# Kernel tuning notes

Hardware: AMD Instinct MI355X
Metric: run time of the kernel (lower is better)

Reference implementation:

```python
import jax, jax.numpy as jnp
import numpy as np

B, T, E, H = 1024, 200, 128, 128
N_ITEMS, N_CATS = 100000, 1000
LN_EPS = 1e-5


def _prelu(x, a):
    return jnp.where(x >= 0, x, a * x)


def _layernorm(x, g, b):
    m = x.mean(-1, keepdims=True)
    v = ((x - m) ** 2).mean(-1, keepdims=True)
    return (x - m) / jnp.sqrt(v + LN_EPS) * g + b


def setup_inputs() -> dict:
    key = jax.random.key(0)
    it = iter(jax.random.split(key, 64))
    nx = lambda: next(it)
    def lin(out_d, in_d):
        s = 1.0 / np.sqrt(in_d)
        return jax.random.uniform(nx(), (out_d, in_d), jnp.float32, -s, s)
    inp = {}
    inp['behavior_ids'] = jax.random.randint(nx(), (B, T), 0, N_ITEMS)
    inp['candidate_id'] = jax.random.randint(nx(), (B,), 0, N_ITEMS)
    inp['candidate_cat'] = jax.random.randint(nx(), (B,), 0, N_CATS)
    inp['dense_features'] = jax.random.normal(nx(), (B, 5), jnp.float32)
    inp['item_emb'] = (jax.random.normal(nx(), (N_ITEMS, E), jnp.float32) * 0.01).at[0].set(0.0)
    inp['cat_emb'] = (jax.random.normal(nx(), (N_CATS, E // 2), jnp.float32) * 0.01).at[0].set(0.0)
    # nn.GRU params (gate order r,z,n)
    inp['gru_wih'] = lin(3 * H, E)
    inp['gru_whh'] = lin(3 * H, H)
    inp['gru_bih'] = jnp.zeros((3 * H,), jnp.float32)
    inp['gru_bhh'] = jnp.zeros((3 * H,), jnp.float32)
    # auxiliary_net: Linear(H,E) -> ReLU -> Linear(E,1)
    inp['aux_w1'] = lin(E, H); inp['aux_b1'] = jnp.zeros((E,), jnp.float32)
    inp['aux_w2'] = lin(1, E); inp['aux_b2'] = jnp.zeros((1,), jnp.float32)
    # attention_mlp: Linear(3H,64) -> PReLU -> Linear(64,1)
    inp['att_w1'] = lin(64, 3 * H); inp['att_b1'] = jnp.zeros((64,), jnp.float32)
    inp['att_a'] = jnp.array(0.25, jnp.float32)
    inp['att_w2'] = lin(1, 64); inp['att_b2'] = jnp.zeros((1,), jnp.float32)
    # AUGRU gates: Linear(2H, H) each
    inp['wz'] = lin(H, 2 * H); inp['bz'] = jnp.zeros((H,), jnp.float32)
    inp['wr'] = lin(H, 2 * H); inp['br'] = jnp.zeros((H,), jnp.float32)
    inp['wh'] = lin(H, 2 * H); inp['bh'] = jnp.zeros((H,), jnp.float32)
    # dense_proj Linear(5,32)
    inp['dp_w'] = lin(32, 5); inp['dp_b'] = jnp.zeros((32,), jnp.float32)
    # MLP: 352 -> 256 -> 128 -> 64, each Linear + LayerNorm + PReLU
    dims = [H + E + E // 2 + 32, 256, 128, 64]
    for i in range(3):
        inp[f'm_w{i+1}'] = lin(dims[i + 1], dims[i])
        inp[f'm_b{i+1}'] = jnp.zeros((dims[i + 1],), jnp.float32)
        inp[f'ln_g{i+1}'] = jnp.ones((dims[i + 1],), jnp.float32)
        inp[f'ln_b{i+1}'] = jnp.zeros((dims[i + 1],), jnp.float32)
        inp[f'pa{i+1}'] = jnp.array(0.25, jnp.float32)
    # 3 task heads Linear(64,1), stacked
    inp['heads_w'] = lin(3, 64); inp['heads_b'] = jnp.zeros((3,), jnp.float32)
    return inp


def _forward_core(behavior_ids, candidate_id, candidate_cat, dense_features,
                  item_emb, cat_emb, gru_wih, gru_whh, gru_bih, gru_bhh,
                  aux_w1, aux_b1, aux_w2, aux_b2,
                  att_w1, att_b1, att_a, att_w2, att_b2,
                  wz, bz, wr, br, wh, bh, dp_w, dp_b,
                  m_w1, m_b1, ln_g1, ln_b1, pa1,
                  m_w2, m_b2, ln_g2, ln_b2, pa2,
                  m_w3, m_b3, ln_g3, ln_b3, pa3,
                  heads_w, heads_b):
    beh = item_emb[behavior_ids]            # [B,T,E]
    cand = item_emb[candidate_id]           # [B,E]
    catv = cat_emb[candidate_cat]           # [B,E//2]
    Bsz = beh.shape[0]
    Hd = gru_whh.shape[1]
    h0 = jnp.zeros((Bsz, Hd), beh.dtype)
    # --- interest extractor GRU (cuDNN GRU math, gate order r,z,n) ---
    xp = jnp.einsum('bte,ge->btg', beh, gru_wih) + gru_bih  # [B,T,3H]
    def gru_step(h, x):
        hp = h @ gru_whh.T + gru_bhh
        xr, xz, xn = jnp.split(x, 3, -1)
        hr, hz, hn = jnp.split(hp, 3, -1)
        r = jax.nn.sigmoid(xr + hr)
        z = jax.nn.sigmoid(xz + hz)
        n = jnp.tanh(xn + r * hn)
        hnew = (1 - z) * n + z * h
        return hnew, hnew
    _, hs = jax.lax.scan(gru_step, h0, jnp.swapaxes(xp, 0, 1))
    hs = jnp.swapaxes(hs, 0, 1)             # [B,T,H]
    # --- auxiliary logits ---
    aux = jax.nn.relu(hs[:, :-1] @ aux_w1.T + aux_b1) @ aux_w2.T + aux_b2  # [B,T-1,1]
    # --- attention (embed_dim == hidden_size so cand_proj == candidate_emb) ---
    ce = cand[:, None, :]
    att_in = jnp.concatenate([hs, jnp.broadcast_to(ce, hs.shape), hs * ce], -1)  # [B,T,3H]
    scores = (_prelu(att_in @ att_w1.T + att_b1, att_a) @ att_w2.T + att_b2)[..., 0]
    att = jax.nn.softmax(scores, axis=-1)   # [B,T]
    # --- AUGRU: attention-modulated update gate ---
    def augru_step(h, xs):
        x, a = xs                           # x: [B,H], a: [B]
        comb = jnp.concatenate([x, h], -1)
        z = jax.nn.sigmoid(comb @ wz.T + bz)
        r = jax.nn.sigmoid(comb @ wr.T + br)
        comb_r = jnp.concatenate([x, r * h], -1)
        ht = jnp.tanh(comb_r @ wh.T + bh)
        zp = a[:, None] * z
        return (1 - zp) * h + zp * ht, None
    hT, _ = jax.lax.scan(augru_step, h0, (jnp.swapaxes(hs, 0, 1), att.T))
    # --- fusion MLP (dropout is identity in eval) ---
    dense_out = dense_features @ dp_w.T + dp_b
    x = jnp.concatenate([hT, cand, catv, dense_out], -1)  # [B,352]
    for (w, b, g, be, a) in ((m_w1, m_b1, ln_g1, ln_b1, pa1),
                             (m_w2, m_b2, ln_g2, ln_b2, pa2),
                             (m_w3, m_b3, ln_g3, ln_b3, pa3)):
        x = _prelu(_layernorm(x @ w.T + b, g, be), a)
    preds = jax.nn.sigmoid(x @ heads_w.T + heads_b)  # [B,3] == 3 heads of [B,1]
    return preds, aux


def reference(behavior_ids, candidate_id, candidate_cat, dense_features,
              item_emb, cat_emb, gru_wih, gru_whh, gru_bih, gru_bhh,
              aux_w1, aux_b1, aux_w2, aux_b2,
              att_w1, att_b1, att_a, att_w2, att_b2,
              wz, bz, wr, br, wh, bh, dp_w, dp_b,
              m_w1, m_b1, ln_g1, ln_b1, pa1,
              m_w2, m_b2, ln_g2, ln_b2, pa2,
              m_w3, m_b3, ln_g3, ln_b3, pa3,
              heads_w, heads_b):
    return _forward_core(behavior_ids, candidate_id, candidate_cat, dense_features,
                         item_emb, cat_emb, gru_wih, gru_whh, gru_bih, gru_bhh,
                         aux_w1, aux_b1, aux_w2, aux_b2,
                         att_w1, att_b1, att_a, att_w2, att_b2,
                         wz, bz, wr, br, wh, bh, dp_w, dp_b,
                         m_w1, m_b1, ln_g1, ln_b1, pa1,
                         m_w2, m_b2, ln_g2, ln_b2, pa2,
                         m_w3, m_b3, ln_g3, ln_b3, pa3,
                         heads_w, heads_b)
```

## Files before the change

kernel.cpp:

```cpp
#include <hip/hip_runtime.h>


typedef __bf16 bf16;
typedef float f32x4 __attribute__((ext_vector_type(4)));
typedef __bf16 bf16x8 __attribute__((ext_vector_type(8)));
typedef __bf16 bf16x4 __attribute__((ext_vector_type(4)));

#define MFMA16(a, b, c) __builtin_amdgcn_mfma_f32_16x16x32_bf16((a), (b), (c), 0, 0, 0)

#define BATCH 1024
#define SEQT 200
#define F32_ONE 0x3F800000u

__device__ __forceinline__ float sigm(float x) {
  return __builtin_amdgcn_rcpf(1.0f + __expf(-x));
}
__device__ __forceinline__ float tanh_fast(float x) {
  float ax = fabsf(x);
  float t = 1.0f - 2.0f * __builtin_amdgcn_rcpf(__expf(2.0f * ax) + 1.0f);
  return copysignf(t, x);
}

__device__ __forceinline__ void bar_lgkm() {
  asm volatile("s_waitcnt lgkmcnt(0)\n\ts_barrier" ::: "memory");
}

__device__ __forceinline__ void dma16(const void* g, void* l) {
  __builtin_amdgcn_global_load_lds((__attribute__((address_space(1))) void*)g,
                                   (__attribute__((address_space(3))) void*)l,
                                   16, 0, 0);
}

template <typename DT> __device__ __forceinline__ float ldf(const DT* p, long i);
template <> __device__ __forceinline__ float ldf<bf16>(const bf16* p, long i) { return (float)p[i]; }
template <> __device__ __forceinline__ float ldf<float>(const float* p, long i) { return p[i]; }

template <typename DT> __device__ __forceinline__ bf16x8 ld8(const DT* p, long i);
template <> __device__ __forceinline__ bf16x8 ld8<bf16>(const bf16* p, long i) {
  return *(const bf16x8*)(p + i);
}
template <> __device__ __forceinline__ bf16x8 ld8<float>(const float* p, long i) {
  f32x4 a = *(const f32x4*)(p + i);
  f32x4 b = *(const f32x4*)(p + i + 4);
  bf16x8 r;
  r[0] = (bf16)a[0]; r[1] = (bf16)a[1]; r[2] = (bf16)a[2]; r[3] = (bf16)a[3];
  r[4] = (bf16)b[0]; r[5] = (bf16)b[1]; r[6] = (bf16)b[2]; r[7] = (bf16)b[3];
  return r;
}

template <typename DT>
__device__ __forceinline__ void cast_body(const DT* __restrict__ src, bf16* __restrict__ dst) {
  const long i = ((long)blockIdx.x * 256 + threadIdx.x) * 8;
  if (i < 100000L * 128) *(bf16x8*)(dst + i) = ld8(src, i);
}
__global__ __launch_bounds__(256) void k_cast(
    const unsigned* __restrict__ disc, const void* src, bf16* dst) {
  if (*disc == F32_ONE) cast_body<float>((const float*)src, dst);
  else                  cast_body<bf16>((const bf16*)src, dst);
}

template <typename DT>
__device__ __forceinline__ void prep_body(
    const int* __restrict__ cid, const int* __restrict__ ccat,
    const DT* __restrict__ dense, const DT* __restrict__ item_emb,
    const DT* __restrict__ cat_emb, const DT* __restrict__ dp_w,
    const DT* __restrict__ dp_b, bf16* __restrict__ candbuf, bf16* __restrict__ xf) {
  const int b = blockIdx.x;
  const int t = threadIdx.x;
  bf16 v = (bf16)ldf(item_emb, (long)cid[b] * 128 + t);
  candbuf[b * 128 + t] = v;
  xf[(long)b * 352 + 128 + t] = v;
  if (t < 64) xf[(long)b * 352 + 256 + t] = (bf16)ldf(cat_emb, (long)ccat[b] * 64 + t);
  if (t < 32) {
    float s = ldf(dp_b, t);
    for (int k = 0; k < 5; k++) s += ldf(dense, b * 5 + k) * ldf(dp_w, t * 5 + k);
    xf[(long)b * 352 + 320 + t] = (bf16)s;
  }
}
__global__ __launch_bounds__(128) void k_prep(
    const unsigned* __restrict__ disc, const int* cid, const int* ccat,
    const void* dense, const void* item_emb, const void* cat_emb,
    const void* dp_w, const void* dp_b, bf16* candbuf, bf16* xf) {
  if (*disc == F32_ONE)
    prep_body<float>(cid, ccat, (const float*)dense, (const float*)item_emb,
                     (const float*)cat_emb, (const float*)dp_w, (const float*)dp_b, candbuf, xf);
  else
    prep_body<bf16>(cid, ccat, (const bf16*)dense, (const bf16*)item_emb,
                    (const bf16*)cat_emb, (const bf16*)dp_w, (const bf16*)dp_b, candbuf, xf);
}

template <typename DT>
__device__ __forceinline__ void gru5_body(
    const int* __restrict__ ids, const bf16* __restrict__ ieb,
    const DT* __restrict__ wih, const DT* __restrict__ whh,
    const DT* __restrict__ bih, const DT* __restrict__ bhh, bf16* __restrict__ hs,
    bf16 (*hA)[16][136], bf16 (*xb)[4][16][128]) {
  const int b0 = blockIdx.x * 16;
  const int tid = threadIdx.x;
  const int w = tid >> 6, lane = tid & 63, l15 = lane & 15, quad = lane >> 4;
  const int nc = w * 16 + l15;

  for (int i = tid; i < 2 * 16 * 136; i += 512) ((bf16*)hA)[i] = (bf16)0.0f;

  bf16x8 wir[4], wiz[4], win_[4], whr[4], whz[4], whn[4];
#pragma unroll
  for (int k = 0; k < 4; k++) {
    const long off = k * 32 + quad * 8;
    wir[k] = ld8(wih, (long)nc * 128 + off);
    wiz[k] = ld8(wih, (long)(128 + nc) * 128 + off);
    win_[k] = ld8(wih, (long)(256 + nc) * 128 + off);
    whr[k] = ld8(whh, (long)nc * 128 + off);
    whz[k] = ld8(whh, (long)(128 + nc) * 128 + off);
    whn[k] = ld8(whh, (long)(256 + nc) * 128 + off);
  }
  const float br_s = ldf(bih, nc) + ldf(bhh, nc);
  const float bz_s = ldf(bih, 128 + nc) + ldf(bhh, 128 + nc);
  const float bxn_s = ldf(bih, 256 + nc);
  const float bhn_s = ldf(bhh, 256 + nc);

  const int idrow = (tid >> 4) & 15;
  const int* idbase = ids + (long)(b0 + idrow) * SEQT;
  const int srcoff = ((tid & 15) ^ (idrow & 7)) * 8;

  auto DMA = [&](const int4 id4, int buf) {
#pragma unroll
    for (int j = 0; j < 2; j++) {
      const int slot = j * 2 + (tid >> 8);
      dma16(ieb + (long)((&id4.x)[slot]) * 128 + srcoff,
            (char*)&xb[buf][0][0][0] + (j * 512 + tid) * 16);
    }
  };

  const int srow = tid >> 5, sch = (tid & 31) * 4;
  bf16* hsb = hs + ((long)(b0 + srow) * SEQT) * 128 + sch;

  float hreg[4] = {0.f, 0.f, 0.f, 0.f};
  const f32x4 z4 = {0.f, 0.f, 0.f, 0.f};

  int4 idv = *(const int4*)(idbase);
  DMA(idv, 0);
  idv = *(const int4*)(idbase + 4);
  asm volatile("s_waitcnt vmcnt(1)" ::: "memory");
  __builtin_amdgcn_sched_barrier(0);
  __builtin_amdgcn_s_barrier();

#define GRU_STEP(P, S, WAITC)                                                  \
  {                                                                            \
    const int tt = t0 + (S);                                                   \
    bf16x8 af[4], xaf[4];                                                      \
    _Pragma("unroll") for (int k = 0; k < 4; k++) {                            \
      af[k] = *(const bf16x8*)&hA[P][l15][k * 32 + quad * 8];                  \
      xaf[k] = *(const bf16x8*)((const char*)&xb[buf][S][0][0] + l15 * 256 +   \
                                ((((k << 2) + quad) ^ (l15 & 7)) << 4));       \
    }                                                                          \
    { const int slot = tt ? tt - 1 : 0;                                        \
      bf16x4 hv = *(const bf16x4*)&hA[P][srow][sch];                           \
      *(bf16x4*)(hsb + (long)slot * 128) = hv; }                               \
    f32x4 ar = z4, az = z4, axn = z4, ahn = z4;                                \
    _Pragma("unroll") for (int k = 0; k < 4; k++) {                            \
      ar = MFMA16(xaf[k], wir[k], ar);                                         \
      az = MFMA16(xaf[k], wiz[k], az);                                         \
      axn = MFMA16(xaf[k], win_[k], axn);                                      \
    }                                                                          \
    _Pragma("unroll") for (int k = 0; k < 4; k++) {                            \
      ar = MFMA16(af[k], whr[k], ar);                                          \
      az = MFMA16(af[k], whz[k], az);                                          \
      ahn = MFMA16(af[k], whn[k], ahn);                                        \
    }                                                                          \
    _Pragma("unroll") for (int r = 0; r < 4; r++) {                            \
      float r_ = sigm(ar[r] + br_s);                                           \
      float z_ = sigm(az[r] + bz_s);                                           \
      float n_ = tanh_fast(axn[r] + bxn_s + r_ * (ahn[r] + bhn_s));            \
      float hnew = (1.0f - z_) * n_ + z_ * hreg[r];                            \
      hreg[r] = hnew;                                                          \
      hA[(P) ^ 1][quad * 4 + r][nc] = (bf16)hnew;                              \
    }                                                                          \
    if (WAITC) {                                                               \
       \
      asm volatile("s_waitcnt vmcnt(5) lgkmcnt(0)\n\ts_barrier" ::: "memory"); \
    } else {                                                                   \
      bar_lgkm();                                                              \
    }                                                                          \
  }

  for (int c = 0; c < 50; c++) {
    const int t0 = c * 4;
    const int buf = c & 1;
    if (c < 49) {
      DMA(idv, buf ^ 1);
      int nid = (c + 2) * 4; if (nid > 196) nid = 196;
      idv = *(const int4*)(idbase + nid);
    }
    GRU_STEP(0, 0, 0) GRU_STEP(1, 1, 0) GRU_STEP(0, 2, 0) GRU_STEP(1, 3, (c < 49))
  }
#undef GRU_STEP
  { bf16x4 hv = *(const bf16x4*)&hA[0][srow][sch];
    *(bf16x4*)(hsb + (long)(SEQT - 1) * 128) = hv; }
}
__global__ __launch_bounds__(512, 1) void k_gru5(
    const unsigned* __restrict__ disc, const int* ids, const bf16* ieb,
    const void* wih, const void* whh, const void* bih, const void* bhh, bf16* hs) {
  __shared__ __align__(16) bf16 hA[2][16][136];
  __shared__ __align__(16) bf16 xb[2][4][16][128];
  if (*disc == F32_ONE)
    gru5_body<float>(ids, ieb, (const float*)wih, (const float*)whh,
                     (const float*)bih, (const float*)bhh, hs, hA, xb);
  else
    gru5_body<bf16>(ids, ieb, (const bf16*)wih, (const bf16*)whh,
                    (const bf16*)bih, (const bf16*)bhh, hs, hA, xb);
}

template <typename DT>
__device__ __forceinline__ void attaux_body(
    const bf16* __restrict__ hs, const int* __restrict__ cid,
    const DT* __restrict__ item_emb,
    const DT* __restrict__ aw1, const DT* __restrict__ ab1,
    const DT* __restrict__ aw2, const DT* __restrict__ ab2,
    const DT* __restrict__ tw1, const DT* __restrict__ tb1, const DT* __restrict__ ta,
    const DT* __restrict__ tw2, const DT* __restrict__ tb2,
    float* __restrict__ sc, float* __restrict__ outaux,
    bf16 (*As)[64][128], float (*scPt)[64], float (*scPa)[64]) {
  const int t0 = blockIdx.x * 64;
  const int b0 = blockIdx.y * 16;
  const int tid = threadIdx.x, w = tid >> 6, lane = tid & 63, l15 = lane & 15, quad = lane >> 4;

  const int tn = w * 16 + l15;
  bf16x8 wth[4], wtc[4], wthc[4], wa0[4], wa1[4];
#pragma unroll
  for (int k = 0; k < 4; k++) {
    const long off = k * 32 + quad * 8;
    wth[k]  = ld8(tw1, (long)tn * 384 + off);
    wtc[k]  = ld8(tw1, (long)tn * 384 + 128 + off);
    wthc[k] = ld8(tw1, (long)tn * 384 + 256 + off);
    wa0[k]  = ld8(aw1, (long)((2 * w) * 16 + l15) * 128 + off);
    wa1[k]  = ld8(aw1, (long)((2 * w + 1) * 16 + l15) * 128 + off);
  }
  const float tb1c = ldf(tb1, tn), tw2c = ldf(tw2, tn);
  const float ab1c0 = ldf(ab1, (2 * w) * 16 + l15), aw2c0 = ldf(aw2, (2 * w) * 16 + l15);
  const float ab1c1 = ldf(ab1, (2 * w + 1) * 16 + l15), aw2c1 = ldf(aw2, (2 * w + 1) * 16 + l15);
  const float aP = ldf(ta, 0), tb2s = ldf(tb2, 0), ab2s = ldf(ab2, 0);

  auto DMA = [&](int b, int buf) {
#pragma unroll
    for (int c = 0; c < 4; c++) {
      const int idx = c * 256 + tid;
      const int row = idx >> 4, p = idx & 15;
      int t = t0 + row; if (t > SEQT - 1) t = SEQT - 1;
      const bf16* src = hs + ((long)b * SEQT + t) * 128 + ((p ^ (row & 7)) * 8);
      dma16(src, (char*)(&As[buf][0][0]) + idx * 16);
    }
  };
  auto CANDLD = [&](int b, bf16x8* cf) {
#pragma unroll
    for (int k = 0; k < 4; k++)
      cf[k] = ld8(item_emb, (long)cid[b] * 128 + k * 32 + quad * 8);
  };

  const f32x4 z4 = {0.f, 0.f, 0.f, 0.f};
  bf16x8 candA[4], candB[4];
  DMA(b0, 0);
  CANDLD(b0, candA);
  asm volatile("s_waitcnt vmcnt(0)" ::: "memory");
  __builtin_amdgcn_sched_barrier(0);
  __builtin_amdgcn_s_barrier();

#define AA_STEP(BI, CUSE, CPF)                                                 \
  {                                                                            \
    const int b = b0 + (BI);                                                   \
    const int buf = (BI) & 1;                                                  \
    if ((BI) + 1 < 16) { DMA(b + 1, buf ^ 1); CANDLD(b + 1, CPF); }            \
    _Pragma("unroll") for (int m = 0; m < 4; m++) {                            \
      const bf16* arow = &As[buf][m * 16 + l15][0];                            \
      bf16x8 af[4], hcf[4];                                                    \
      _Pragma("unroll") for (int k = 0; k < 4; k++)                            \
        af[k] = *(const bf16x8*)((const char*)arow +                           \
                                 (((k * 4 + quad) ^ (l15 & 7)) << 4));         \
      _Pragma("unroll") for (int k = 0; k < 4; k++)                            \
      _Pragma("unroll") for (int j = 0; j < 8; j++)                            \
        hcf[k][j] = (bf16)((float)af[k][j] * (float)CUSE[k][j]);               \
      f32x4 at = z4, aa0 = z4, aa1 = z4;                                       \
      _Pragma("unroll") for (int k = 0; k < 4; k++) {                          \
        at = MFMA16(af[k], wth[k], at);                                        \
        at = MFMA16(CUSE[k], wtc[k], at);                                      \
        at = MFMA16(hcf[k], wthc[k], at);                                      \
        aa0 = MFMA16(af[k], wa0[k], aa0);                                      \
        aa1 = MFMA16(af[k], wa1[k], aa1);                                      \
      }                                                                        \
      float tp[4], ap[4];                                                      \
      _Pragma("unroll") for (int r = 0; r < 4; r++) {                          \
        float y = at[r] + tb1c;                                                \
        y = (y >= 0.f) ? y : aP * y;                                           \
        tp[r] = y * tw2c;                                                      \
        float y0 = aa0[r] + ab1c0;                                             \
        float y1 = aa1[r] + ab1c1;                                             \
        ap[r] = (y0 > 0.f ? y0 : 0.f) * aw2c0 + (y1 > 0.f ? y1 : 0.f) * aw2c1; \
      }                                                                        \
      _Pragma("unroll") for (int mm = 1; mm < 16; mm <<= 1)                    \
      _Pragma("unroll") for (int r = 0; r < 4; r++) {                          \
        tp[r] += __shfl_xor(tp[r], mm, 64);                                    \
        ap[r] += __shfl_xor(ap[r], mm, 64);                                    \
      }                                                                        \
      if (l15 == 0) {                                                          \
        *(float4*)&scPt[w][m * 16 + quad * 4] =                                \
            make_float4(tp[0], tp[1], tp[2], tp[3]);                           \
        *(float4*)&scPa[w][m * 16 + quad * 4] =                                \
            make_float4(ap[0], ap[1], ap[2], ap[3]);                           \
      }                                                                        \
    }                                                                          \
    bar_lgkm();                                                                \
    if (tid < 64) {                                                            \
      int t = t0 + tid;                                                        \
      if (t < SEQT) {                                                          \
        float s = scPt[0][tid] + scPt[1][tid] + scPt[2][tid] + scPt[3][tid];   \
        sc[(long)b * SEQT + t] = s + tb2s;                                     \
      }                                                                        \
    } else if (tid < 128) {                                                    \
      int tt2 = tid - 64, t = t0 + tt2;                                        \
      if (t < SEQT - 1) {                                                      \
        float s = scPa[0][tt2] + scPa[1][tt2] + scPa[2][tt2] + scPa[3][tt2];   \
        outaux[(long)b * 199 + t] = s + ab2s;                                  \
      }                                                                        \
    }                                                                          \
    asm volatile("s_waitcnt vmcnt(0) lgkmcnt(0)" ::: "memory");                \
    __builtin_amdgcn_sched_barrier(0);                                         \
    __builtin_amdgcn_s_barrier();                                              \
  }

  for (int bi = 0; bi < 16; bi += 2) {
    AA_STEP(bi, candA, candB)
    AA_STEP(bi + 1, candB, candA)
  }
#undef AA_STEP
}
__global__ __launch_bounds__(256, 1) void k_attaux(
    const unsigned* __restrict__ disc, const bf16* hs, const int* cid,
    const void* item_emb,
    const void* aw1, const void* ab1, const void* aw2, const void* ab2,
    const void* tw1, const void* tb1, const void* ta, const void* tw2, const void* tb2,
    float* sc, float* outaux) {
  __shared__ __align__(16) bf16 As[2][64][128];
  __shared__ __align__(16) float scPt[4][64];
  __shared__ __align__(16) float scPa[4][64];
  if (*disc == F32_ONE)
    attaux_body<float>(hs, cid, (const float*)item_emb,
                       (const float*)aw1, (const float*)ab1, (const float*)aw2, (const float*)ab2,
                       (const float*)tw1, (const float*)tb1, (const float*)ta,
                       (const float*)tw2, (const float*)tb2, sc, outaux, As, scPt, scPa);
  else
    attaux_body<bf16>(hs, cid, (const bf16*)item_emb,
                      (const bf16*)aw1, (const bf16*)ab1, (const bf16*)aw2, (const bf16*)ab2,
                      (const bf16*)tw1, (const bf16*)tb1, (const bf16*)ta,
                      (const bf16*)tw2, (const bf16*)tb2, sc, outaux, As, scPt, scPa);
}

__global__ __launch_bounds__(256) void k_softmax(float* __restrict__ sc) {
  const int b = blockIdx.x, tid = threadIdx.x;
  __shared__ float red[256];
  float v = (tid < SEQT) ? sc[(long)b * SEQT + tid] : -1e30f;
  red[tid] = v; __syncthreads();
  for (int s = 128; s > 0; s >>= 1) { if (tid < s) red[tid] = fmaxf(red[tid], red[tid + s]); __syncthreads(); }
  float mx = red[0]; __syncthreads();
  float e = (tid < SEQT) ? __expf(v - mx) : 0.f;
  red[tid] = e; __syncthreads();
  for (int s = 128; s > 0; s >>= 1) { if (tid < s) red[tid] += red[tid + s]; __syncthreads(); }
  float inv = 1.0f / red[0];
  if (tid < SEQT) sc[(long)b * SEQT + tid] = e * inv;
}

template <typename DT>
__device__ __forceinline__ void augru5_body(
    const bf16* __restrict__ hsrc, const float* __restrict__ att,
    const DT* __restrict__ wz, const DT* __restrict__ wr, const DT* __restrict__ wh,
    const DT* __restrict__ bzv, const DT* __restrict__ brv, const DT* __restrict__ bhv,
    bf16* __restrict__ xf_out,
    bf16 (*hA)[16][136], bf16 (*rhA)[136], float (*attL)[201],
    bf16 (*xb)[4][16][128]) {
  const int b0 = blockIdx.x * 16;
  const int tid = threadIdx.x;
  const int w = tid >> 6, lane = tid & 63, l15 = lane & 15, quad = lane >> 4;
  const int nc = w * 16 + l15;

  for (int i = tid; i < 2 * 16 * 136; i += 512) ((bf16*)hA)[i] = (bf16)0.0f;
  for (int i = tid; i < 16 * SEQT; i += 512) {
    int r = i / SEQT, c = i - r * SEQT;
    attL[r][c] = att[(long)(b0 + r) * SEQT + c];
  }

  bf16x8 wzx[4], wzh[4], wrx[4], wrh[4], whx[4], whh_[4];
#pragma unroll
  for (int k = 0; k < 4; k++) {
    const long off = k * 32 + quad * 8;
    wzx[k] = ld8(wz, (long)nc * 256 + off);
    wzh[k] = ld8(wz, (long)nc * 256 + 128 + off);
    wrx[k] = ld8(wr, (long)nc * 256 + off);
    wrh[k] = ld8(wr, (long)nc * 256 + 128 + off);
    whx[k] = ld8(wh, (long)nc * 256 + off);
    whh_[k] = ld8(wh, (long)nc * 256 + 128 + off);
  }
  const float bz_s = ldf(bzv, nc);
  const float br_s = ldf(brv, nc);
  const float bh_s = ldf(bhv, nc);

  const int drow = (tid >> 4) & 15;
  const int srcoff = ((tid & 15) ^ (drow & 7)) * 8;
  auto DMA = [&](int t0, int buf) {
#pragma unroll
    for (int j = 0; j < 2; j++) {
      const int slot = j * 2 + (tid >> 8);
      dma16(hsrc + ((long)(b0 + drow) * SEQT + t0 + slot) * 128 + srcoff,
            (char*)&xb[buf][0][0][0] + (j * 512 + tid) * 16);
    }
  };

  float hreg[4] = {0.f, 0.f, 0.f, 0.f};
  const f32x4 z4 = {0.f, 0.f, 0.f, 0.f};

  DMA(0, 0);
  asm volatile("s_waitcnt vmcnt(0)" ::: "memory");
  __builtin_amdgcn_sched_barrier(0);
  __builtin_amdgcn_s_barrier();

#define AUGRU_STEP(P, S, WAITC)                                                \
  {                                                                            \
    const int tt = t0 + (S);                                                   \
    bf16x8 af[4], xaf[4];                                                      \
    _Pragma("unroll") for (int k = 0; k < 4; k++) {                            \
      af[k] = *(const bf16x8*)&hA[P][l15][k * 32 + quad * 8];                  \
      xaf[k] = *(const bf16x8*)((const char*)&xb[buf][S][0][0] + l15 * 256 +   \
                                ((((k << 2) + quad) ^ (l15 & 7)) << 4));       \
    }                                                                          \
    f32x4 az = z4, ar = z4, axh = z4;                                          \
    _Pragma("unroll") for (int k = 0; k < 4; k++) {                            \
      az = MFMA16(xaf[k], wzx[k], az);                                         \
      ar = MFMA16(xaf[k], wrx[k], ar);                                         \
      axh = MFMA16(xaf[k], whx[k], axh);                                       \
    }                                                                          \
    _Pragma("unroll") for (int k = 0; k < 4; k++) {                            \
      az = MFMA16(af[k], wzh[k], az);                                          \
      ar = MFMA16(af[k], wrh[k], ar);                                          \
    }                                                                          \
    float zp[4];                                                               \
    _Pragma("unroll") for (int r = 0; r < 4; r++) {                            \
      float a_ = attL[quad * 4 + r][tt];                                       \
      float z_ = sigm(az[r] + bz_s);                                           \
      float r_ = sigm(ar[r] + br_s);                                           \
      zp[r] = a_ * z_;                                                         \
      rhA[quad * 4 + r][nc] = (bf16)(r_ * hreg[r]);                            \
    }                                                                          \
    bar_lgkm();                                                                \
    bf16x8 rf[4];                                                              \
    _Pragma("unroll") for (int k = 0; k < 4; k++)                              \
      rf[k] = *(const bf16x8*)&rhA[l15][k * 32 + quad * 8];                    \
    f32x4 ahh = axh;                                                           \
    _Pragma("unroll") for (int k = 0; k < 4; k++)                              \
      ahh = MFMA16(rf[k], whh_[k], ahh);                                       \
    _Pragma("unroll") for (int r = 0; r < 4; r++) {                            \
      float ht = tanh_fast(ahh[r] + bh_s);                                     \
      float hnew = (1.f - zp[r]) * hreg[r] + zp[r] * ht;                       \
      hreg[r] = hnew;                                                          \
      hA[(P) ^ 1][quad * 4 + r][nc] = (bf16)hnew;                              \
    }                                                                          \
    if (WAITC) {                                                               \
                     \
      asm volatile("s_waitcnt vmcnt(0) lgkmcnt(0)\n\ts_barrier" ::: "memory"); \
    } else {                                                                   \
      bar_lgkm();                                                              \
    }                                                                          \
  }

  for (int c = 0; c < 50; c++) {
    const int t0 = c * 4;
    const int buf = c & 1;
    if (c < 49) DMA((c + 1) * 4, buf ^ 1);
    AUGRU_STEP(0, 0, 0) AUGRU_STEP(1, 1, 0) AUGRU_STEP(0, 2, 0) AUGRU_STEP(1, 3, (c < 49))
  }
#undef AUGRU_STEP
#pragma unroll
  for (int r = 0; r < 4; r++)
    xf_out[(long)(b0 + quad * 4 + r) * 352 + nc] = (bf16)hreg[r];
}
__global__ __launch_bounds__(512, 1) void k_augru5(
    const unsigned* __restrict__ disc, const bf16* hsrc, const float* att,
    const void* wz, const void* wr, const void* wh,
    const void* bzv, const void* brv, const void* bhv, bf16* xf_out) {
  __shared__ __align__(16) bf16 hA[2][16][136];
  __shared__ __align__(16) bf16 rhA[16][136];
  __shared__ __align__(16) float attL[16][201];
  __shared__ __align__(16) bf16 xb[2][4][16][128];
  if (*disc == F32_ONE)
    augru5_body<float>(hsrc, att, (const float*)wz, (const float*)wr, (const float*)wh,
                       (const float*)bzv, (const float*)brv, (const float*)bhv, xf_out,
                       hA, rhA, attL, xb);
  else
    augru5_body<bf16>(hsrc, att, (const bf16*)wz, (const bf16*)wr, (const bf16*)wh,
                      (const bf16*)bzv, (const bf16*)brv, (const bf16*)bhv, xf_out,
                      hA, rhA, attL, xb);
}

template <typename DT>
__device__ __forceinline__ void mlp_body(
    const bf16* __restrict__ xf,
    const DT* __restrict__ w1, const DT* __restrict__ b1, const DT* __restrict__ g1, const DT* __restrict__ be1, const DT* __restrict__ pa1,
    const DT* __restrict__ w2, const DT* __restrict__ b2, const DT* __restrict__ g2, const DT* __restrict__ be2, const DT* __restrict__ pa2,
    const DT* __restrict__ w3, const DT* __restrict__ b3, const DT* __restrict__ g3, const DT* __restrict__ be3, const DT* __restrict__ pa3,
    const DT* __restrict__ hw, const DT* __restrict__ hb, float* __restrict__ preds,
    float (*xs)[352], float (*ys)[256]) {
  const int tid = threadIdx.x, w = tid >> 6, lane = tid & 63;
  const int b = blockIdx.x * 4 + w;
  for (int i = lane; i < 352; i += 64) xs[w][i] = (float)xf[(long)b * 352 + i];
  __syncthreads();
  float acc1[4];
#pragma unroll
  for (int oi = 0; oi < 4; oi++) {
    int o = lane + 64 * oi;
    float s = ldf(b1, o);
    for (int k = 0; k < 352; k += 8) {
      bf16x8 wv = ld8(w1, (long)o * 352 + k);
#pragma unroll
      for (int j = 0; j < 8; j++) s += xs[w][k + j] * (float)wv[j];
    }
    acc1[oi] = s;
  }
  float sm = acc1[0] + acc1[1] + acc1[2] + acc1[3];
#pragma unroll
  for (int m = 1; m < 64; m <<= 1) sm += __shfl_xor(sm, m, 64);
  float mean = sm * (1.0f / 256.0f);
  float vs = 0.f;
#pragma unroll
  for (int oi = 0; oi < 4; oi++) { float d = acc1[oi] - mean; vs += d * d; }
#pragma unroll
  for (int m = 1; m < 64; m <<= 1) vs += __shfl_xor(vs, m, 64);
  float rstd = rsqrtf(vs * (1.0f / 256.0f) + 1e-5f);
  float a1 = ldf(pa1, 0);
#pragma unroll
  for (int oi = 0; oi < 4; oi++) {
    int o = lane + 64 * oi;
    float y = (acc1[oi] - mean) * rstd * ldf(g1, o) + ldf(be1, o);
    ys[w][o] = (y >= 0.f) ? y : a1 * y;
  }
  __syncthreads();
  float acc2[2];
#pragma unroll
  for (int oi = 0; oi < 2; oi++) {
    int o = lane + 64 * oi;
    float s = ldf(b2, o);
    for (int k = 0; k < 256; k += 8) {
      bf16x8 wv = ld8(w2, (long)o * 256 + k);
#pragma unroll
      for (int j = 0; j < 8; j++) s += ys[w][k + j] * (float)wv[j];
    }
    acc2[oi] = s;
  }
  sm = acc2[0] + acc2[1];
#pragma unroll
  for (int m = 1; m < 64; m <<= 1) sm += __shfl_xor(sm, m, 64);
  mean = sm * (1.0f / 128.0f);
  vs = 0.f;
#pragma unroll
  for (int oi = 0; oi < 2; oi++) { float d = acc2[oi] - mean; vs += d * d; }
#pragma unroll
  for (int m = 1; m < 64; m <<= 1) vs += __shfl_xor(vs, m, 64);
  rstd = rsqrtf(vs * (1.0f / 128.0f) + 1e-5f);
  float a2 = ldf(pa2, 0);
  __syncthreads();
#pragma unroll
  for (int oi = 0; oi < 2; oi++) {
    int o = lane + 64 * oi;
    float y = (acc2[oi] - mean) * rstd * ldf(g2, o) + ldf(be2, o);
    xs[w][o] = (y >= 0.f) ? y : a2 * y;
  }
  __syncthreads();
  float s3 = ldf(b3, lane);
  for (int k = 0; k < 128; k += 8) {
    bf16x8 wv = ld8(w3, (long)lane * 128 + k);
#pragma unroll
    for (int j = 0; j < 8; j++) s3 += xs[w][k + j] * (float)wv[j];
  }
  sm = s3;
#pragma unroll
  for (int m = 1; m < 64; m <<= 1) sm += __shfl_xor(sm, m, 64);
  mean = sm * (1.0f / 64.0f);
  float d3 = s3 - mean;
  vs = d3 * d3;
#pragma unroll
  for (int m = 1; m < 64; m <<= 1) vs += __shfl_xor(vs, m, 64);
  rstd = rsqrtf(vs * (1.0f / 64.0f) + 1e-5f);
  float a3 = ldf(pa3, 0);
  float y3 = d3 * rstd * ldf(g3, lane) + ldf(be3, lane);
  y3 = (y3 >= 0.f) ? y3 : a3 * y3;
  ys[w][lane] = y3;
  __syncthreads();
  if (lane < 3) {
    float s = ldf(hb, lane);
    for (int k = 0; k < 64; k++) s += ys[w][k] * ldf(hw, lane * 64 + k);
    preds[(long)b * 3 + lane] = sigm(s);
  }
}
__global__ __launch_bounds__(256) void k_mlp(
    const unsigned* __restrict__ disc, const bf16* xf,
    const void* w1, const void* b1, const void* g1, const void* be1, const void* pa1,
    const void* w2, const void* b2, const void* g2, const void* be2, const void* pa2,
    const void* w3, const void* b3, const void* g3, const void* be3, const void* pa3,
    const void* hw, const void* hb, float* preds) {
  __shared__ float xs[4][352];
  __shared__ float ys[4][256];
  if (*disc == F32_ONE)
    mlp_body<float>(xf,
        (const float*)w1, (const float*)b1, (const float*)g1, (const float*)be1, (const float*)pa1,
        (const float*)w2, (const float*)b2, (const float*)g2, (const float*)be2, (const float*)pa2,
        (const float*)w3, (const float*)b3, (const float*)g3, (const float*)be3, (const float*)pa3,
        (const float*)hw, (const float*)hb, preds, xs, ys);
  else
    mlp_body<bf16>(xf,
        (const bf16*)w1, (const bf16*)b1, (const bf16*)g1, (const bf16*)be1, (const bf16*)pa1,
        (const bf16*)w2, (const bf16*)b2, (const bf16*)g2, (const bf16*)be2, (const bf16*)pa2,
        (const bf16*)w3, (const bf16*)b3, (const bf16*)g3, (const bf16*)be3, (const bf16*)pa3,
        (const bf16*)hw, (const bf16*)hb, preds, xs, ys);
}

extern "C" void kernel_launch(void* const* d_in, const int* in_sizes, int n_in,
                              void* d_out, int out_size, void* d_ws, size_t ws_size,
                              hipStream_t stream) {
  const int* behavior_ids = (const int*)d_in[0];
  const int* candidate_id = (const int*)d_in[1];
  const int* candidate_cat = (const int*)d_in[2];
  const void* dense = d_in[3];
  const void* item_emb = d_in[4];
  const void* cat_emb = d_in[5];
  const void* gru_wih = d_in[6];
  const void* gru_whh = d_in[7];
  const void* gru_bih = d_in[8];
  const void* gru_bhh = d_in[9];
  const void* aux_w1 = d_in[10];
  const void* aux_b1 = d_in[11];
  const void* aux_w2 = d_in[12];
  const void* aux_b2 = d_in[13];
  const void* att_w1 = d_in[14];
  const void* att_b1 = d_in[15];
  const void* att_a = d_in[16];
  const void* att_w2 = d_in[17];
  const void* att_b2 = d_in[18];
  const void* wz = d_in[19];
  const void* bz = d_in[20];
  const void* wr = d_in[21];
  const void* br = d_in[22];
  const void* wh = d_in[23];
  const void* bh = d_in[24];
  const void* dp_w = d_in[25];
  const void* dp_b = d_in[26];
  const void* m_w1 = d_in[27];
  const void* m_b1 = d_in[28];
  const void* ln_g1 = d_in[29];
  const void* ln_b1 = d_in[30];
  const void* pa1 = d_in[31];
  const void* m_w2 = d_in[32];
  const void* m_b2 = d_in[33];
  const void* ln_g2 = d_in[34];
  const void* ln_b2 = d_in[35];
  const void* pa2 = d_in[36];
  const void* m_w3 = d_in[37];
  const void* m_b3 = d_in[38];
  const void* ln_g3 = d_in[39];
  const void* ln_b3 = d_in[40];
  const void* pa3 = d_in[41];
  const void* heads_w = d_in[42];
  const void* heads_b = d_in[43];
  (void)in_sizes; (void)n_in; (void)out_size; (void)ws_size;

  const unsigned* disc = (const unsigned*)ln_g1;

  char* ws = (char*)d_ws;
  bf16* HS = (bf16*)(ws);
  float* SC = (float*)(ws + 52428800L);
  bf16* CAND = (bf16*)(ws + 53248000L);
  bf16* XF = (bf16*)(ws + 53510144L);
  bf16* IEB = (bf16*)(ws + 54231040L);
  float* OUT = (float*)d_out;

  k_cast<<<6250, 256, 0, stream>>>(disc, item_emb, IEB);
  k_prep<<<BATCH, 128, 0, stream>>>(disc, candidate_id, candidate_cat, dense, item_emb,
                                    cat_emb, dp_w, dp_b, CAND, XF);
  k_gru5<<<64, 512, 0, stream>>>(disc, behavior_ids, IEB, gru_wih, gru_whh,
                                 gru_bih, gru_bhh, HS);
  k_attaux<<<dim3(4, 64), 256, 0, stream>>>(disc, HS, candidate_id, item_emb,
                                            aux_w1, aux_b1, aux_w2, aux_b2,
                                            att_w1, att_b1, att_a, att_w2, att_b2,
                                            SC, OUT + 3072);
  k_softmax<<<BATCH, 256, 0, stream>>>(SC);
  k_augru5<<<64, 512, 0, stream>>>(disc, HS, SC, wz, wr, wh, bz, br, bh, XF);
  k_mlp<<<256, 256, 0, stream>>>(disc, XF,
      m_w1, m_b1, ln_g1, ln_b1, pa1,
      m_w2, m_b2, ln_g2, ln_b2, pa2,
      m_w3, m_b3, ln_g3, ln_b3, pa3,
      heads_w, heads_b, OUT);
}
```

Before: 733.9 us.

## Precompute next-step input projections in GRU/AUGRU and merge init kernels

In both the GRU and AUGRU recurrences, the input-projection MFMAs for step t+1 are issued right after step t's gate math, so they can overlap with the hidden-state dependency chain instead of sitting on the serial critical path. The cast and prep kernels are merged into one launch, and the unused candidate buffer is dropped. In the attention/aux kernel, the per-block barrier waits with vmcnt(4) instead of a full vmcnt(0) drain when more blocks follow. This costs extra live accumulator registers and adds risk if the partial vmcnt wait does not match the outstanding load count.

```diff
diff --git a/kernel.cpp b/kernel.cpp
--- a/kernel.cpp
+++ b/kernel.cpp
@@ -49,48 +49,43 @@
 }
 
 template <typename DT>
-__device__ __forceinline__ void cast_body(const DT* __restrict__ src, bf16* __restrict__ dst) {
-  const long i = ((long)blockIdx.x * 256 + threadIdx.x) * 8;
-  if (i < 100000L * 128) *(bf16x8*)(dst + i) = ld8(src, i);
-}
-__global__ __launch_bounds__(256) void k_cast(
-    const unsigned* __restrict__ disc, const void* src, bf16* dst) {
-  if (*disc == F32_ONE) cast_body<float>((const float*)src, dst);
-  else                  cast_body<bf16>((const bf16*)src, dst);
+__device__ __forceinline__ void init_body(
+    const DT* __restrict__ item_emb, bf16* __restrict__ ieb,
+    const int* __restrict__ cid, const int* __restrict__ ccat,
+    const DT* __restrict__ dense, const DT* __restrict__ cat_emb,
+    const DT* __restrict__ dp_w, const DT* __restrict__ dp_b,
+    bf16* __restrict__ xf) {
+  if (blockIdx.x < 6250) {
+    const long i = ((long)blockIdx.x * 256 + threadIdx.x) * 8;
+    if (i < 100000L * 128) *(bf16x8*)(ieb + i) = ld8(item_emb, i);
+    return;
+  }
+  const int b = blockIdx.x - 6250;
+  const int t = threadIdx.x;
+  if (t < 128) {
+    xf[(long)b * 352 + 128 + t] = (bf16)ldf(item_emb, (long)cid[b] * 128 + t);
+    if (t < 64) xf[(long)b * 352 + 256 + t] = (bf16)ldf(cat_emb, (long)ccat[b] * 64 + t);
+    if (t < 32) {
+      float s = ldf(dp_b, t);
+      for (int k = 0; k < 5; k++) s += ldf(dense, b * 5 + k) * ldf(dp_w, t * 5 + k);
+      xf[(long)b * 352 + 320 + t] = (bf16)s;
+    }
+  }
+}
+__global__ __launch_bounds__(256) void k_init(
+    const unsigned* __restrict__ disc, const void* item_emb, bf16* ieb,
+    const int* cid, const int* ccat, const void* dense, const void* cat_emb,
+    const void* dp_w, const void* dp_b, bf16* xf) {
+  if (*disc == F32_ONE)
+    init_body<float>((const float*)item_emb, ieb, cid, ccat, (const float*)dense,
+                     (const float*)cat_emb, (const float*)dp_w, (const float*)dp_b, xf);
+  else
+    init_body<bf16>((const bf16*)item_emb, ieb, cid, ccat, (const bf16*)dense,
+                    (const bf16*)cat_emb, (const bf16*)dp_w, (const bf16*)dp_b, xf);
 }
 
 template <typename DT>
-__device__ __forceinline__ void prep_body(
-    const int* __restrict__ cid, const int* __restrict__ ccat,
-    const DT* __restrict__ dense, const DT* __restrict__ item_emb,
-    const DT* __restrict__ cat_emb, const DT* __restrict__ dp_w,
-    const DT* __restrict__ dp_b, bf16* __restrict__ candbuf, bf16* __restrict__ xf) {
-  const int b = blockIdx.x;
-  const int t = threadIdx.x;
-  bf16 v = (bf16)ldf(item_emb, (long)cid[b] * 128 + t);
-  candbuf[b * 128 + t] = v;
-  xf[(long)b * 352 + 128 + t] = v;
-  if (t < 64) xf[(long)b * 352 + 256 + t] = (bf16)ldf(cat_emb, (long)ccat[b] * 64 + t);
-  if (t < 32) {
-    float s = ldf(dp_b, t);
-    for (int k = 0; k < 5; k++) s += ldf(dense, b * 5 + k) * ldf(dp_w, t * 5 + k);
-    xf[(long)b * 352 + 320 + t] = (bf16)s;
-  }
-}
-__global__ __launch_bounds__(128) void k_prep(
-    const unsigned* __restrict__ disc, const int* cid, const int* ccat,
-    const void* dense, const void* item_emb, const void* cat_emb,
-    const void* dp_w, const void* dp_b, bf16* candbuf, bf16* xf) {
-  if (*disc == F32_ONE)
-    prep_body<float>(cid, ccat, (const float*)dense, (const float*)item_emb,
-                     (const float*)cat_emb, (const float*)dp_w, (const float*)dp_b, candbuf, xf);
-  else
-    prep_body<bf16>(cid, ccat, (const bf16*)dense, (const bf16*)item_emb,
-                    (const bf16*)cat_emb, (const bf16*)dp_w, (const bf16*)dp_b, candbuf, xf);
-}
-
-template <typename DT>
-__device__ __forceinline__ void gru5_body(
+__device__ __forceinline__ void gru9_body(
     const int* __restrict__ ids, const bf16* __restrict__ ieb,
     const DT* __restrict__ wih, const DT* __restrict__ whh,
     const DT* __restrict__ bih, const DT* __restrict__ bhh, bf16* __restrict__ hs,
@@ -118,9 +113,9 @@
   const float bxn_s = ldf(bih, 256 + nc);
   const float bhn_s = ldf(bhh, 256 + nc);
 
-  const int idrow = (tid >> 4) & 15;
-  const int* idbase = ids + (long)(b0 + idrow) * SEQT;
-  const int srcoff = ((tid & 15) ^ (idrow & 7)) * 8;
+  const int drow = (tid >> 4) & 15;
+  const int* idbase = ids + (long)(b0 + drow) * SEQT;
+  const int srcoff = ((tid & 15) ^ (drow & 7)) * 8;
 
   auto DMA = [&](const int4 id4, int buf) {
 #pragma unroll
@@ -136,6 +131,7 @@
 
   float hreg[4] = {0.f, 0.f, 0.f, 0.f};
   const f32x4 z4 = {0.f, 0.f, 0.f, 0.f};
+  f32x4 pxr = z4, pxz = z4, pxn = z4;
 
   int4 idv = *(const int4*)(idbase);
   DMA(idv, 0);
@@ -144,23 +140,31 @@
   __builtin_amdgcn_sched_barrier(0);
   __builtin_amdgcn_s_barrier();
 
-#define GRU_STEP(P, S, WAITC)                                                  \
+#define XLD(DST, BUF, SS)                                                      \
+  _Pragma("unroll") for (int k = 0; k < 4; k++)                                \
+    DST[k] = *(const bf16x8*)((const char*)&xb[BUF][SS][0][0] + l15 * 256 +    \
+                              ((((k << 2) + quad) ^ (l15 & 7)) << 4));
+
+#define GRU_STEP(P, S, PRE, DOPRE, WAITC)                                      \
   {                                                                            \
     const int tt = t0 + (S);                                                   \
-    bf16x8 af[4], xaf[4];                                                      \
-    _Pragma("unroll") for (int k = 0; k < 4; k++) {                            \
+    bf16x8 af[4];                                                              \
+    _Pragma("unroll") for (int k = 0; k < 4; k++)                              \
       af[k] = *(const bf16x8*)&hA[P][l15][k * 32 + quad * 8];                  \
-      xaf[k] = *(const bf16x8*)((const char*)&xb[buf][S][0][0] + l15 * 256 +   \
-                                ((((k << 2) + quad) ^ (l15 & 7)) << 4));       \
-    }                                                                          \
     { const int slot = tt ? tt - 1 : 0;                                        \
       bf16x4 hv = *(const bf16x4*)&hA[P][srow][sch];                           \
       *(bf16x4*)(hsb + (long)slot * 128) = hv; }                               \
-    f32x4 ar = z4, az = z4, axn = z4, ahn = z4;                                \
-    _Pragma("unroll") for (int k = 0; k < 4; k++) {                            \
-      ar = MFMA16(xaf[k], wir[k], ar);                                         \
-      az = MFMA16(xaf[k], wiz[k], az);                                         \
-      axn = MFMA16(xaf[k], win_[k], axn);                                      \
+    f32x4 ar, az, axn, ahn = z4;                                               \
+    if (PRE) { ar = pxr; az = pxz; axn = pxn; }                                \
+    else {                                                                     \
+      bf16x8 xaf[4];                                                           \
+      XLD(xaf, buf, S)                                                         \
+      ar = z4; az = z4; axn = z4;                                              \
+      _Pragma("unroll") for (int k = 0; k < 4; k++) {                          \
+        ar = MFMA16(xaf[k], wir[k], ar);                                       \
+        az = MFMA16(xaf[k], wiz[k], az);                                       \
+        axn = MFMA16(xaf[k], win_[k], axn);                                    \
+      }                                                                        \
     }                                                                          \
     _Pragma("unroll") for (int k = 0; k < 4; k++) {                            \
       ar = MFMA16(af[k], whr[k], ar);                                          \
@@ -174,6 +178,16 @@
       float hnew = (1.0f - z_) * n_ + z_ * hreg[r];                            \
       hreg[r] = hnew;                                                          \
       hA[(P) ^ 1][quad * 4 + r][nc] = (bf16)hnew;                              \
+    }                                                                          \
+    if (DOPRE) {                                                               \
+      bf16x8 xafN[4];                                                          \
+      XLD(xafN, buf, (S) + 1)                                                  \
+      pxr = z4; pxz = z4; pxn = z4;                                            \
+      _Pragma("unroll") for (int k = 0; k < 4; k++) {                          \
+        pxr = MFMA16(xafN[k], wir[k], pxr);                                    \
+        pxz = MFMA16(xafN[k], wiz[k], pxz);                                    \
+        pxn = MFMA16(xafN[k], win_[k], pxn);                                   \
+      }                                                                        \
     }                                                                          \
     if (WAITC) {                                                               \
        \
@@ -191,22 +205,23 @@
       int nid = (c + 2) * 4; if (nid > 196) nid = 196;
       idv = *(const int4*)(idbase + nid);
     }
-    GRU_STEP(0, 0, 0) GRU_STEP(1, 1, 0) GRU_STEP(0, 2, 0) GRU_STEP(1, 3, (c < 49))
+    GRU_STEP(0, 0, 0, 1, 0) GRU_STEP(1, 1, 1, 1, 0)
+    GRU_STEP(0, 2, 1, 1, 0) GRU_STEP(1, 3, 1, 0, (c < 49))
   }
 #undef GRU_STEP
   { bf16x4 hv = *(const bf16x4*)&hA[0][srow][sch];
     *(bf16x4*)(hsb + (long)(SEQT - 1) * 128) = hv; }
 }
-__global__ __launch_bounds__(512, 1) void k_gru5(
+__global__ __launch_bounds__(512, 1) void k_gru9(
     const unsigned* __restrict__ disc, const int* ids, const bf16* ieb,
     const void* wih, const void* whh, const void* bih, const void* bhh, bf16* hs) {
   __shared__ __align__(16) bf16 hA[2][16][136];
   __shared__ __align__(16) bf16 xb[2][4][16][128];
   if (*disc == F32_ONE)
-    gru5_body<float>(ids, ieb, (const float*)wih, (const float*)whh,
+    gru9_body<float>(ids, ieb, (const float*)wih, (const float*)whh,
                      (const float*)bih, (const float*)bhh, hs, hA, xb);
   else
-    gru5_body<bf16>(ids, ieb, (const bf16*)wih, (const bf16*)whh,
+    gru9_body<bf16>(ids, ieb, (const bf16*)wih, (const bf16*)whh,
                     (const bf16*)bih, (const bf16*)bhh, hs, hA, xb);
 }
 
@@ -321,9 +336,12 @@
         outaux[(long)b * 199 + t] = s + ab2s;                                  \
       }                                                                        \
     }                                                                          \
-    asm volatile("s_waitcnt vmcnt(0) lgkmcnt(0)" ::: "memory");                \
-    __builtin_amdgcn_sched_barrier(0);                                         \
-    __builtin_amdgcn_s_barrier();                                              \
+    if ((BI) + 1 < 16) {                                                       \
+             \
+      asm volatile("s_waitcnt vmcnt(4) lgkmcnt(0)\n\ts_barrier" ::: "memory"); \
+    } else {                                                                   \
+      asm volatile("s_waitcnt vmcnt(0) lgkmcnt(0)\n\ts_barrier" ::: "memory"); \
+    }                                                                          \
   }
 
   for (int bi = 0; bi < 16; bi += 2) {
@@ -368,7 +386,7 @@
 }
 
 template <typename DT>
-__device__ __forceinline__ void augru5_body(
+__device__ __forceinline__ void augru9_body(
     const bf16* __restrict__ hsrc, const float* __restrict__ att,
     const DT* __restrict__ wz, const DT* __restrict__ wr, const DT* __restrict__ wh,
     const DT* __restrict__ bzv, const DT* __restrict__ brv, const DT* __restrict__ bhv,
@@ -414,26 +432,30 @@
 
   float hreg[4] = {0.f, 0.f, 0.f, 0.f};
   const f32x4 z4 = {0.f, 0.f, 0.f, 0.f};
+  f32x4 pxz = z4, pxr = z4, pxh = z4;
 
   DMA(0, 0);
   asm volatile("s_waitcnt vmcnt(0)" ::: "memory");
   __builtin_amdgcn_sched_barrier(0);
   __builtin_amdgcn_s_barrier();
 
-#define AUGRU_STEP(P, S, WAITC)                                                \
+#define AUGRU_STEP(P, S, PRE, DOPRE, WAITC)                                    \
   {                                                                            \
     const int tt = t0 + (S);                                                   \
-    bf16x8 af[4], xaf[4];                                                      \
-    _Pragma("unroll") for (int k = 0; k < 4; k++) {                            \
+    bf16x8 af[4];                                                              \
+    _Pragma("unroll") for (int k = 0; k < 4; k++)                              \
       af[k] = *(const bf16x8*)&hA[P][l15][k * 32 + quad * 8];                  \
-      xaf[k] = *(const bf16x8*)((const char*)&xb[buf][S][0][0] + l15 * 256 +   \
-                                ((((k << 2) + quad) ^ (l15 & 7)) << 4));       \
-    }                                                                          \
-    f32x4 az = z4, ar = z4, axh = z4;                                          \
-    _Pragma("unroll") for (int k = 0; k < 4; k++) {                            \
-      az = MFMA16(xaf[k], wzx[k], az);                                         \
-      ar = MFMA16(xaf[k], wrx[k], ar);                                         \
-      axh = MFMA16(xaf[k], whx[k], axh);                                       \
+    f32x4 az, ar, axh;                                                         \
+    if (PRE) { az = pxz; ar = pxr; axh = pxh; }                                \
+    else {                                                                     \
+      bf16x8 xaf[4];                                                           \
+      XLD(xaf, buf, S)                                                         \
+      az = z4; ar = z4; axh = z4;                                              \
+      _Pragma("unroll") for (int k = 0; k < 4; k++) {                          \
+        az = MFMA16(xaf[k], wzx[k], az);                                       \
+        ar = MFMA16(xaf[k], wrx[k], ar);                                       \
+        axh = MFMA16(xaf[k], whx[k], axh);                                     \
+      }                                                                        \
     }                                                                          \
     _Pragma("unroll") for (int k = 0; k < 4; k++) {                            \
       az = MFMA16(af[k], wzh[k], az);                                          \
@@ -446,6 +468,16 @@
       float r_ = sigm(ar[r] + br_s);                                           \
       zp[r] = a_ * z_;                                                         \
       rhA[quad * 4 + r][nc] = (bf16)(r_ * hreg[r]);                            \
+    }                                                                          \
+    if (DOPRE) {                                                               \
+      bf16x8 xafN[4];                                                          \
+      XLD(xafN, buf, (S) + 1)                                                  \
+      pxz = z4; pxr = z4; pxh = z4;                                            \
+      _Pragma("unroll") for (int k = 0; k < 4; k++) {                          \
+        pxz = MFMA16(xafN[k], wzx[k], pxz);                                    \
+        pxr = MFMA16(xafN[k], wrx[k], pxr);                                    \
+        pxh = MFMA16(xafN[k], whx[k], pxh);                                    \
+      }                                                                        \
     }                                                                          \
     bar_lgkm();                                                                \
     bf16x8 rf[4];                                                              \
@@ -472,14 +504,15 @@
     const int t0 = c * 4;
     const int buf = c & 1;
     if (c < 49) DMA((c + 1) * 4, buf ^ 1);
-    AUGRU_STEP(0, 0, 0) AUGRU_STEP(1, 1, 0) AUGRU_STEP(0, 2, 0) AUGRU_STEP(1, 3, (c < 49))
+    AUGRU_STEP(0, 0, 0, 1, 0) AUGRU_STEP(1, 1, 1, 1, 0)
+    AUGRU_STEP(0, 2, 1, 1, 0) AUGRU_STEP(1, 3, 1, 0, (c < 49))
   }
 #undef AUGRU_STEP
 #pragma unroll
   for (int r = 0; r < 4; r++)
     xf_out[(long)(b0 + quad * 4 + r) * 352 + nc] = (bf16)hreg[r];
 }
-__global__ __launch_bounds__(512, 1) void k_augru5(
+__global__ __launch_bounds__(512, 1) void k_augru9(
     const unsigned* __restrict__ disc, const bf16* hsrc, const float* att,
     const void* wz, const void* wr, const void* wh,
     const void* bzv, const void* brv, const void* bhv, bf16* xf_out) {
@@ -488,11 +521,11 @@
   __shared__ __align__(16) float attL[16][201];
   __shared__ __align__(16) bf16 xb[2][4][16][128];
   if (*disc == F32_ONE)
-    augru5_body<float>(hsrc, att, (const float*)wz, (const float*)wr, (const float*)wh,
+    augru9_body<float>(hsrc, att, (const float*)wz, (const float*)wr, (const float*)wh,
                        (const float*)bzv, (const float*)brv, (const float*)bhv, xf_out,
                        hA, rhA, attL, xb);
   else
-    augru5_body<bf16>(hsrc, att, (const bf16*)wz, (const bf16*)wr, (const bf16*)wh,
+    augru9_body<bf16>(hsrc, att, (const bf16*)wz, (const bf16*)wr, (const bf16*)wh,
                       (const bf16*)bzv, (const bf16*)brv, (const bf16*)bhv, xf_out,
                       hA, rhA, attL, xb);
 }
@@ -672,22 +705,20 @@
   char* ws = (char*)d_ws;
   bf16* HS = (bf16*)(ws);
   float* SC = (float*)(ws + 52428800L);
-  bf16* CAND = (bf16*)(ws + 53248000L);
   bf16* XF = (bf16*)(ws + 53510144L);
   bf16* IEB = (bf16*)(ws + 54231040L);
   float* OUT = (float*)d_out;
 
-  k_cast<<<6250, 256, 0, stream>>>(disc, item_emb, IEB);
-  k_prep<<<BATCH, 128, 0, stream>>>(disc, candidate_id, candidate_cat, dense, item_emb,
-                                    cat_emb, dp_w, dp_b, CAND, XF);
-  k_gru5<<<64, 512, 0, stream>>>(disc, behavior_ids, IEB, gru_wih, gru_whh,
+  k_init<<<6250 + BATCH, 256, 0, stream>>>(disc, item_emb, IEB, candidate_id,
+                                           candidate_cat, dense, cat_emb, dp_w, dp_b, XF);
+  k_gru9<<<64, 512, 0, stream>>>(disc, behavior_ids, IEB, gru_wih, gru_whh,
                                  gru_bih, gru_bhh, HS);
   k_attaux<<<dim3(4, 64), 256, 0, stream>>>(disc, HS, candidate_id, item_emb,
                                             aux_w1, aux_b1, aux_w2, aux_b2,
                                             att_w1, att_b1, att_a, att_w2, att_b2,
                                             SC, OUT + 3072);
   k_softmax<<<BATCH, 256, 0, stream>>>(SC);
-  k_augru5<<<64, 512, 0, stream>>>(disc, HS, SC, wz, wr, wh, bz, br, bh, XF);
+  k_augru9<<<64, 512, 0, stream>>>(disc, HS, SC, wz, wr, wh, bz, br, bh, XF);
   k_mlp<<<256, 256, 0, stream>>>(disc, XF,
       m_w1, m_b1, ln_g1, ln_b1, pa1,
       m_w2, m_b2, ln_g2, ln_b2, pa2,
```

Measured after the change: 727.4 us. About the same (-0.9%).
